# Kernel optimization log

Hardware: AMD Instinct MI355X
Metric: run time of the kernel (lower is better)

## Reference

```python
import jax, jax.numpy as jnp
import numpy as np

IN_DIM = 2048
OUT_DIM = 2048
GRID_SIZE = 8
BATCH = 4096
LN_EPS = 1e-5


def setup_inputs() -> dict:
    key = jax.random.key(0)
    k_x, k_w = jax.random.split(key)
    x = jax.random.normal(k_x, (BATCH, IN_DIM), dtype=jnp.float32)
    spline_weight = jax.random.normal(k_w, (OUT_DIM, IN_DIM, GRID_SIZE), dtype=jnp.float32) * 0.1
    return {
        "x": x,
        "ln_weight": jnp.ones((IN_DIM,), jnp.float32),
        "ln_bias": jnp.zeros((IN_DIM,), jnp.float32),
        "spline_weight": spline_weight,
        "scale_base": jnp.ones((OUT_DIM, IN_DIM), jnp.float32),
        "bias": jnp.zeros((OUT_DIM,), jnp.float32),
        "rbf_beta": jnp.full((1,), 2.0, jnp.float32),
        "grid": jnp.linspace(-1.0, 1.0, GRID_SIZE, dtype=jnp.float32),
    }


def reference(x, ln_weight, ln_bias, spline_weight, scale_base, bias, rbf_beta, grid):
    # LayerNorm over last dim (eps=1e-5, elementwise affine)
    mu = jnp.mean(x, axis=-1, keepdims=True)
    var = jnp.mean(jnp.square(x - mu), axis=-1, keepdims=True)
    xn = (x - mu) * jax.lax.rsqrt(var + LN_EPS) * ln_weight + ln_bias  # (B, in)

    beta = jnp.clip(rbf_beta, 0.5, 6.0)  # (1,)
    # RBF basis: (B, in, G)
    basis = jnp.exp(-jnp.square(xn[..., None] - grid) * beta)

    # Torch einsum('bdig,oid->bod') broadcasts the singleton d of basis against
    # spline_weight's last axis and sums g; after .sum(-1) this equals
    # (sum_g basis) @ (sum_d spline_weight).T
    S = basis.sum(-1)              # (B, in)
    Wd = spline_weight.sum(-1)     # (out, in)
    spline_sum = jnp.einsum('bi,oi->bo', S, Wd)

    base_out = jnp.einsum('bi,oi->bo', xn, scale_base)
    return base_out + spline_sum + bias
```

## Files before the change

kernel.cpp:

```cpp
#include <hip/hip_runtime.h>
#include <hip/hip_bf16.h>
#include <stdint.h>

constexpr int IN_DIM   = 2048;
constexpr int OUT_DIM  = 2048;
constexpr int BATCH    = 4096;
constexpr int KDIM     = 2 * IN_DIM;
constexpr float LN_EPS = 1e-5f;

#define TILE 128
#define BK   32

typedef __attribute__((ext_vector_type(8))) short  short8;
typedef __attribute__((ext_vector_type(4))) float  f32x4;

__device__ __forceinline__ unsigned short f2bf(float f) {
  __hip_bfloat16 h = __float2bfloat16(f);
  return *reinterpret_cast<unsigned short*>(&h);
}

__global__ __launch_bounds__(256) void ln_rbf_kernel(
    const float* __restrict__ x, const float* __restrict__ lnw,
    const float* __restrict__ lnb, const float* __restrict__ betap,
    const float* __restrict__ grid, unsigned short* __restrict__ A)
{
  const int row = blockIdx.x;
  const int tid = threadIdx.x;
  const float4* xr = reinterpret_cast<const float4*>(x + (size_t)row * IN_DIM);
  float4 v0 = xr[tid];
  float4 v1 = xr[tid + 256];
  float s = (v0.x + v0.y) + (v0.z + v0.w) + (v1.x + v1.y) + (v1.z + v1.w);
  float q = v0.x * v0.x + v0.y * v0.y + v0.z * v0.z + v0.w * v0.w
          + v1.x * v1.x + v1.y * v1.y + v1.z * v1.z + v1.w * v1.w;
  #pragma unroll
  for (int off = 32; off > 0; off >>= 1) {
    s += __shfl_down(s, off, 64);
    q += __shfl_down(q, off, 64);
  }
  __shared__ float red[10];
  const int lane = tid & 63, wv = tid >> 6;
  if (lane == 0) { red[wv] = s; red[4 + wv] = q; }
  __syncthreads();
  if (tid == 0) {
    float ts = (red[0] + red[1]) + (red[2] + red[3]);
    float tq = (red[4] + red[5]) + (red[6] + red[7]);
    float mu  = ts * (1.0f / IN_DIM);
    float var = tq * (1.0f / IN_DIM) - mu * mu;
    red[8] = mu;
    red[9] = rsqrtf(var + LN_EPS);
  }
  __syncthreads();
  const float mu = red[8], rs = red[9];
  const float beta = fminf(fmaxf(betap[0], 0.5f), 6.0f);
  float g[8];
  #pragma unroll
  for (int i = 0; i < 8; i++) g[i] = grid[i];
  const float4* w4 = reinterpret_cast<const float4*>(lnw);
  const float4* b4 = reinterpret_cast<const float4*>(lnb);
  unsigned short* Ar = A + (size_t)row * KDIM;
  #pragma unroll
  for (int h = 0; h < 2; h++) {
    const int idx = tid + h * 256;
    float4 xv  = (h == 0) ? v0 : v1;
    float4 wv4 = w4[idx];
    float4 bv4 = b4[idx];
    float xa[4] = {xv.x, xv.y, xv.z, xv.w};
    float wa[4] = {wv4.x, wv4.y, wv4.z, wv4.w};
    float ba[4] = {bv4.x, bv4.y, bv4.z, bv4.w};
    float xn[4], S[4];
    #pragma unroll
    for (int c = 0; c < 4; c++) {
      float xnv = (xa[c] - mu) * rs * wa[c] + ba[c];
      xn[c] = xnv;
      float acc = 0.f;
      #pragma unroll
      for (int gg = 0; gg < 8; gg++) {
        float d = xnv - g[gg];
        acc += __expf(-beta * d * d);
      }
      S[c] = acc;
    }
    uint2 px, ps;
    px.x = (unsigned)f2bf(xn[0]) | ((unsigned)f2bf(xn[1]) << 16);
    px.y = (unsigned)f2bf(xn[2]) | ((unsigned)f2bf(xn[3]) << 16);
    ps.x = (unsigned)f2bf(S[0])  | ((unsigned)f2bf(S[1])  << 16);
    ps.y = (unsigned)f2bf(S[2])  | ((unsigned)f2bf(S[3])  << 16);
    *reinterpret_cast<uint2*>(Ar + idx * 4) = px;
    *reinterpret_cast<uint2*>(Ar + IN_DIM + idx * 4) = ps;
  }
}

__global__ __launch_bounds__(256) void pack_b_kernel(
    const float* __restrict__ sw, const float* __restrict__ sb,
    unsigned short* __restrict__ B)
{
  const int t  = blockIdx.x * 256 + threadIdx.x;
  const int o  = t >> 10;
  const int i0 = (t & 1023) * 2;
  float2 sv = *reinterpret_cast<const float2*>(sb + (size_t)o * IN_DIM + i0);
  unsigned u0 = (unsigned)f2bf(sv.x) | ((unsigned)f2bf(sv.y) << 16);
  *reinterpret_cast<unsigned*>(B + (size_t)o * KDIM + i0) = u0;
  const float4* sp = reinterpret_cast<const float4*>(sw + ((size_t)o * IN_DIM + i0) * 8);
  float4 a0 = sp[0], a1 = sp[1], a2 = sp[2], a3 = sp[3];
  float s0 = ((a0.x + a0.y) + (a0.z + a0.w)) + ((a1.x + a1.y) + (a1.z + a1.w));
  float s1 = ((a2.x + a2.y) + (a2.z + a2.w)) + ((a3.x + a3.y) + (a3.z + a3.w));
  unsigned u1 = (unsigned)f2bf(s0) | ((unsigned)f2bf(s1) << 16);
  *reinterpret_cast<unsigned*>(B + (size_t)o * KDIM + IN_DIM + i0) = u1;
}

__device__ __forceinline__ void gld_lds16(const unsigned short* g, unsigned short* l) {
  __builtin_amdgcn_global_load_lds(
      (const __attribute__((address_space(1))) void*)g,
      (__attribute__((address_space(3))) void*)l, 16, 0, 0);
}

__global__ __launch_bounds__(256) void gemm_kernel(
    const unsigned short* __restrict__ A, const unsigned short* __restrict__ Bm,
    const float* __restrict__ bias, float* __restrict__ out)
{
  __shared__ __align__(16) unsigned short As[TILE * BK];
  __shared__ __align__(16) unsigned short Bs[TILE * BK];
  const int tid  = threadIdx.x;
  const int lane = tid & 63;
  const int wv   = tid >> 6;
  const int wr   = wv >> 1;
  const int wc   = wv & 1;
  const int m0   = blockIdx.y * TILE;
  const int n0   = blockIdx.x * TILE;
  const int lrow = lane & 15;
  const int lk   = (lane >> 4) * 8;

  f32x4 acc[4][4] = {};

  const int seg0 = tid;
  const int r0 = seg0 >> 2, c0 = (seg0 & 3) * 8;
  const int seg1 = 256 + seg0;
  const int r1 = seg1 >> 2, c1 = (seg1 & 3) * 8;
  unsigned short* ldsA0 = &As[(wv * 64) * 8];
  unsigned short* ldsA1 = &As[(256 + wv * 64) * 8];
  unsigned short* ldsB0 = &Bs[(wv * 64) * 8];
  unsigned short* ldsB1 = &Bs[(256 + wv * 64) * 8];
  const unsigned short* Ab = A  + (size_t)(m0 + r0) * KDIM + c0;
  const unsigned short* Ab1= A  + (size_t)(m0 + r1) * KDIM + c1;
  const unsigned short* Bb = Bm + (size_t)(n0 + r0) * KDIM + c0;
  const unsigned short* Bb1= Bm + (size_t)(n0 + r1) * KDIM + c1;

  for (int k0 = 0; k0 < KDIM; k0 += BK) {
    __syncthreads();
    gld_lds16(Ab  + k0, ldsA0);
    gld_lds16(Ab1 + k0, ldsA1);
    gld_lds16(Bb  + k0, ldsB0);
    gld_lds16(Bb1 + k0, ldsB1);
    __syncthreads();

    short8 af[4], bf[4];
    #pragma unroll
    for (int mi = 0; mi < 4; mi++)
      af[mi] = *reinterpret_cast<const short8*>(&As[(wr * 64 + mi * 16 + lrow) * BK + lk]);
    #pragma unroll
    for (int ni = 0; ni < 4; ni++)
      bf[ni] = *reinterpret_cast<const short8*>(&Bs[(wc * 64 + ni * 16 + lrow) * BK + lk]);
    #pragma unroll
    for (int mi = 0; mi < 4; mi++)
      #pragma unroll
      for (int ni = 0; ni < 4; ni++)
        acc[mi][ni] = __builtin_amdgcn_mfma_f32_16x16x32_bf16(af[mi], bf[ni], acc[mi][ni], 0, 0, 0);
  }

  const int rb = (lane >> 4) * 4;
  #pragma unroll
  for (int ni = 0; ni < 4; ni++) {
    const int col = n0 + wc * 64 + ni * 16 + lrow;
    const float bv = bias[col];
    #pragma unroll
    for (int mi = 0; mi < 4; mi++) {
      const int rowm = m0 + wr * 64 + mi * 16 + rb;
      #pragma unroll
      for (int r = 0; r < 4; r++)
        out[(size_t)(rowm + r) * OUT_DIM + col] = acc[mi][ni][r] + bv;
    }
  }
}

extern "C" void kernel_launch(void* const* d_in, const int* in_sizes, int n_in,
                              void* d_out, int out_size, void* d_ws, size_t ws_size,
                              hipStream_t stream) {
  const float* x    = (const float*)d_in[0];
  const float* lnw  = (const float*)d_in[1];
  const float* lnb  = (const float*)d_in[2];
  const float* sw   = (const float*)d_in[3];
  const float* sb   = (const float*)d_in[4];
  const float* bias = (const float*)d_in[5];
  const float* beta = (const float*)d_in[6];
  const float* grid = (const float*)d_in[7];
  float* out = (float*)d_out;

  unsigned short* A = (unsigned short*)d_ws;
  unsigned short* B = A + (size_t)BATCH * KDIM;

  hipLaunchKernelGGL(ln_rbf_kernel, dim3(BATCH), dim3(256), 0, stream,
                     x, lnw, lnb, beta, grid, A);
  hipLaunchKernelGGL(pack_b_kernel, dim3((OUT_DIM * (IN_DIM / 2)) / 256), dim3(256), 0, stream,
                     sw, sb, B);
  hipLaunchKernelGGL(gemm_kernel, dim3(OUT_DIM / TILE, BATCH / TILE), dim3(256), 0, stream,
                     A, B, bias, out);
}
```

Measured before the change: 336.5 us.

## Double GEMM K-tile, XOR-swizzle LDS, and coalesce spline weight packing

The GEMM K tile grows from 32 to 64, halving the number of barrier-separated load/compute iterations. LDS tiles use an XOR swizzle on the 16-byte column chunks so the MFMA fragment reads avoid bank conflicts. The weight packing kernel now has one thread per float4 of spline_weight and reduces pairs with lane shuffles, so the 128 MB weight read is fully coalesced. This adds LDS use (32 KB per block) and more fragment registers, which may lower occupancy.

```diff
diff --git a/kernel.cpp b/kernel.cpp
--- a/kernel.cpp
+++ b/kernel.cpp
@@ -9,7 +9,7 @@
 constexpr float LN_EPS = 1e-5f;
 
 #define TILE 128
-#define BK   32
+#define BK   64
 
 typedef __attribute__((ext_vector_type(8))) short  short8;
 typedef __attribute__((ext_vector_type(4))) float  f32x4;
@@ -17,6 +17,9 @@
 __device__ __forceinline__ unsigned short f2bf(float f) {
   __hip_bfloat16 h = __float2bfloat16(f);
   return *reinterpret_cast<unsigned short*>(&h);
+}
+__device__ __forceinline__ unsigned pack2bf(float a, float b) {
+  return (unsigned)f2bf(a) | ((unsigned)f2bf(b) << 16);
 }
 
 __global__ __launch_bounds__(256) void ln_rbf_kernel(
@@ -81,31 +84,45 @@
       S[c] = acc;
     }
     uint2 px, ps;
-    px.x = (unsigned)f2bf(xn[0]) | ((unsigned)f2bf(xn[1]) << 16);
-    px.y = (unsigned)f2bf(xn[2]) | ((unsigned)f2bf(xn[3]) << 16);
-    ps.x = (unsigned)f2bf(S[0])  | ((unsigned)f2bf(S[1])  << 16);
-    ps.y = (unsigned)f2bf(S[2])  | ((unsigned)f2bf(S[3])  << 16);
+    px.x = pack2bf(xn[0], xn[1]);
+    px.y = pack2bf(xn[2], xn[3]);
+    ps.x = pack2bf(S[0], S[1]);
+    ps.y = pack2bf(S[2], S[3]);
     *reinterpret_cast<uint2*>(Ar + idx * 4) = px;
     *reinterpret_cast<uint2*>(Ar + IN_DIM + idx * 4) = ps;
   }
 }
 
+constexpr int SW_F4   = OUT_DIM * IN_DIM * 2;
+constexpr int SB_F4   = OUT_DIM * IN_DIM / 4;
+
 __global__ __launch_bounds__(256) void pack_b_kernel(
     const float* __restrict__ sw, const float* __restrict__ sb,
-    unsigned short* __restrict__ B)
+    unsigned* __restrict__ Bu)
 {
-  const int t  = blockIdx.x * 256 + threadIdx.x;
-  const int o  = t >> 10;
-  const int i0 = (t & 1023) * 2;
-  float2 sv = *reinterpret_cast<const float2*>(sb + (size_t)o * IN_DIM + i0);
-  unsigned u0 = (unsigned)f2bf(sv.x) | ((unsigned)f2bf(sv.y) << 16);
-  *reinterpret_cast<unsigned*>(B + (size_t)o * KDIM + i0) = u0;
-  const float4* sp = reinterpret_cast<const float4*>(sw + ((size_t)o * IN_DIM + i0) * 8);
-  float4 a0 = sp[0], a1 = sp[1], a2 = sp[2], a3 = sp[3];
-  float s0 = ((a0.x + a0.y) + (a0.z + a0.w)) + ((a1.x + a1.y) + (a1.z + a1.w));
-  float s1 = ((a2.x + a2.y) + (a2.z + a2.w)) + ((a3.x + a3.y) + (a3.z + a3.w));
-  unsigned u1 = (unsigned)f2bf(s0) | ((unsigned)f2bf(s1) << 16);
-  *reinterpret_cast<unsigned*>(B + (size_t)o * KDIM + IN_DIM + i0) = u1;
+  const int g = blockIdx.x * 256 + threadIdx.x;
+  const int lane = threadIdx.x & 63;
+  if (g < SW_F4) {
+    float4 v = reinterpret_cast<const float4*>(sw)[g];
+    float s = (v.x + v.y) + (v.z + v.w);
+    s += __shfl_xor(s, 1, 64);
+    float hi = __shfl_down(s, 2, 64);
+    if ((lane & 3) == 0) {
+      const int i_lin = g >> 1;
+      const int o = i_lin >> 11;
+      const int i = i_lin & (IN_DIM - 1);
+      Bu[(size_t)o * (KDIM / 2) + (IN_DIM / 2) + (i >> 1)] = pack2bf(s, hi);
+    }
+  } else {
+    const int t = g - SW_F4;
+    float4 v = reinterpret_cast<const float4*>(sb)[t];
+    const int o  = t >> 9;
+    const int i4 = t & 511;
+    uint2 u;
+    u.x = pack2bf(v.x, v.y);
+    u.y = pack2bf(v.z, v.w);
+    *reinterpret_cast<uint2*>(&Bu[(size_t)o * (KDIM / 2) + i4 * 2]) = u;
+  }
 }
 
 __device__ __forceinline__ void gld_lds16(const unsigned short* g, unsigned short* l) {
@@ -128,43 +145,57 @@
   const int m0   = blockIdx.y * TILE;
   const int n0   = blockIdx.x * TILE;
   const int lrow = lane & 15;
-  const int lk   = (lane >> 4) * 8;
+  const int lkq  = lane >> 4;
 
   f32x4 acc[4][4] = {};
 
-  const int seg0 = tid;
-  const int r0 = seg0 >> 2, c0 = (seg0 & 3) * 8;
-  const int seg1 = 256 + seg0;
-  const int r1 = seg1 >> 2, c1 = (seg1 & 3) * 8;
-  unsigned short* ldsA0 = &As[(wv * 64) * 8];
-  unsigned short* ldsA1 = &As[(256 + wv * 64) * 8];
-  unsigned short* ldsB0 = &Bs[(wv * 64) * 8];
-  unsigned short* ldsB1 = &Bs[(256 + wv * 64) * 8];
-  const unsigned short* Ab = A  + (size_t)(m0 + r0) * KDIM + c0;
-  const unsigned short* Ab1= A  + (size_t)(m0 + r1) * KDIM + c1;
-  const unsigned short* Bb = Bm + (size_t)(n0 + r0) * KDIM + c0;
-  const unsigned short* Bb1= Bm + (size_t)(n0 + r1) * KDIM + c1;
+  const unsigned short* Ap[4];
+  const unsigned short* Bp[4];
+  unsigned short* ldsA[4];
+  unsigned short* ldsB[4];
+  #pragma unroll
+  for (int j = 0; j < 4; j++) {
+    const int seg  = j * 256 + wv * 64 + lane;
+    const int row  = seg >> 3;
+    const int gcol = ((seg & 7) ^ (row & 7)) * 8;
+    Ap[j] = A  + (size_t)(m0 + row) * KDIM + gcol;
+    Bp[j] = Bm + (size_t)(n0 + row) * KDIM + gcol;
+    ldsA[j] = &As[(j * 256 + wv * 64) * 8];
+    ldsB[j] = &Bs[(j * 256 + wv * 64) * 8];
+  }
 
   for (int k0 = 0; k0 < KDIM; k0 += BK) {
     __syncthreads();
-    gld_lds16(Ab  + k0, ldsA0);
-    gld_lds16(Ab1 + k0, ldsA1);
-    gld_lds16(Bb  + k0, ldsB0);
-    gld_lds16(Bb1 + k0, ldsB1);
+    #pragma unroll
+    for (int j = 0; j < 4; j++) gld_lds16(Ap[j] + k0, ldsA[j]);
+    #pragma unroll
+    for (int j = 0; j < 4; j++) gld_lds16(Bp[j] + k0, ldsB[j]);
     __syncthreads();
 
-    short8 af[4], bf[4];
-    #pragma unroll
-    for (int mi = 0; mi < 4; mi++)
-      af[mi] = *reinterpret_cast<const short8*>(&As[(wr * 64 + mi * 16 + lrow) * BK + lk]);
-    #pragma unroll
-    for (int ni = 0; ni < 4; ni++)
-      bf[ni] = *reinterpret_cast<const short8*>(&Bs[(wc * 64 + ni * 16 + lrow) * BK + lk]);
-    #pragma unroll
-    for (int mi = 0; mi < 4; mi++)
-      #pragma unroll
-      for (int ni = 0; ni < 4; ni++)
-        acc[mi][ni] = __builtin_amdgcn_mfma_f32_16x16x32_bf16(af[mi], bf[ni], acc[mi][ni], 0, 0, 0);
+    short8 af[2][4], bf[2][4];
+    #pragma unroll
+    for (int h = 0; h < 2; h++) {
+      #pragma unroll
+      for (int mi = 0; mi < 4; mi++) {
+        const int r = wr * 64 + mi * 16 + lrow;
+        af[h][mi] = *reinterpret_cast<const short8*>(
+            &As[r * BK + (((h << 2) | lkq) ^ (lrow & 7)) * 8]);
+      }
+      #pragma unroll
+      for (int ni = 0; ni < 4; ni++) {
+        const int r = wc * 64 + ni * 16 + lrow;
+        bf[h][ni] = *reinterpret_cast<const short8*>(
+            &Bs[r * BK + (((h << 2) | lkq) ^ (lrow & 7)) * 8]);
+      }
+    }
+    #pragma unroll
+    for (int h = 0; h < 2; h++)
+      #pragma unroll
+      for (int mi = 0; mi < 4; mi++)
+        #pragma unroll
+        for (int ni = 0; ni < 4; ni++)
+          acc[mi][ni] = __builtin_amdgcn_mfma_f32_16x16x32_bf16(
+              af[h][mi], bf[h][ni], acc[mi][ni], 0, 0, 0);
   }
 
   const int rb = (lane >> 4) * 4;
@@ -200,8 +231,8 @@
 
   hipLaunchKernelGGL(ln_rbf_kernel, dim3(BATCH), dim3(256), 0, stream,
                      x, lnw, lnb, beta, grid, A);
-  hipLaunchKernelGGL(pack_b_kernel, dim3((OUT_DIM * (IN_DIM / 2)) / 256), dim3(256), 0, stream,
-                     sw, sb, B);
+  hipLaunchKernelGGL(pack_b_kernel, dim3((SW_F4 + SB_F4) / 256), dim3(256), 0, stream,
+                     sw, sb, (unsigned*)B);
   hipLaunchKernelGGL(gemm_kernel, dim3(OUT_DIM / TILE, BATCH / TILE), dim3(256), 0, stream,
                      A, B, bias, out);
 }
```

After: 316.8 us. -5.9%, faster.
